# Kernel tuning notes

Hardware: AMD Instinct MI355X
Metric: run time of the kernel (lower is better)

## Reference

```python
import jax, jax.numpy as jnp
import numpy as np

N = 100_000      # nodes
E = 1_600_000    # edges
F_IN = 64        # num_node_features
F = 64           # features_size
OUT = 1          # output_size
V = 2            # variants
A = 6            # activities per variant (second_encoder applied after each)
P = 8192         # (place, src, dst) triples per activity step


def setup_inputs() -> dict:
    key = jax.random.key(0)
    ks = jax.random.split(key, 16)
    s = 1.0 / np.sqrt(F)
    return {
        "x": jax.random.normal(ks[0], (N, F_IN), jnp.float32),
        "edge_index": jax.random.randint(ks[1], (2, E), 0, N, dtype=jnp.int32),
        "places": jax.random.randint(ks[2], (V, A, P), 0, N, dtype=jnp.int32),
        "srcs": jax.random.randint(ks[3], (V, A, P), 0, N, dtype=jnp.int32),
        "dsts": jax.random.randint(ks[4], (V, A, P), 0, N, dtype=jnp.int32),
        "W1": jax.random.normal(ks[5], (F_IN, F), jnp.float32) * s,
        "Wself1": jax.random.normal(ks[6], (F_IN, F), jnp.float32) * s,
        "b1": jnp.zeros((F,), jnp.float32),
        "W2": jax.random.normal(ks[7], (F, F), jnp.float32) * s,
        "Wself2": jax.random.normal(ks[8], (F, F), jnp.float32) * s,
        "b2": jnp.zeros((F,), jnp.float32),
        "Wd1": jax.random.normal(ks[9], (3 * F, F), jnp.float32) * s,
        "bd1": jnp.zeros((F,), jnp.float32),
        "Wd2": jax.random.normal(ks[10], (F, OUT), jnp.float32) * s,
        "bd2": jnp.zeros((OUT,), jnp.float32),
    }


def _gcn(h, edge_src, edge_dst, W, Wself, b):
    # message passing: sum-aggregate neighbor features, then linear + relu
    agg = jax.ops.segment_sum(h[edge_src], edge_dst, num_segments=N)  # [N, F]
    return jax.nn.relu(agg @ W + h @ Wself + b)


def reference(x, edge_index, places, srcs, dsts,
              W1, Wself1, b1, W2, Wself2, b2, Wd1, bd1, Wd2, bd2):
    edge_src, edge_dst = edge_index[0], edge_index[1]

    def decode(feat, p, s, d):
        # gather-concat-MLP-logsigmoid per (place, src, dst) triple
        cat = jnp.concatenate([feat[p], feat[s], feat[d]], axis=-1)  # [P, 3F]
        h = jax.nn.relu(cat @ Wd1 + bd1)
        return jax.nn.log_sigmoid(h @ Wd2 + bd2)                     # [P, OUT]

    feat0 = _gcn(x, edge_src, edge_dst, W1, Wself1, b1)  # first_encoder
    predictions = jnp.zeros((N, OUT), x.dtype)
    for v in range(V):
        feat = feat0  # features reset to post-first-encoder per variant
        pred = jnp.zeros((N, OUT), x.dtype)
        prev_prob = jnp.zeros((OUT,), x.dtype)
        for a in range(A):
            p, s, d = places[v, a], srcs[v, a], dsts[v, a]
            pp = decode(feat, p, s, d)          # [P, OUT]
            pred = pred.at[p].add(pp)           # scatter per place
            prev_prob = prev_prob + pred[p].sum(axis=0)
            pred = pred.at[p].add(prev_prob)    # broadcast to predicted places
            feat = _gcn(feat, edge_src, edge_dst, W2, Wself2, b2)  # second_encoder
        predictions = predictions + pred
    return predictions
```

## Files before the change

kernel.cpp:

```cpp
#include <hip/hip_runtime.h>
#include <hip/hip_bf16.h>

#define F 64
#define VARIANTS 2
#define ACTS 6


__global__ void k_hist(const int* __restrict__ dst, int* __restrict__ deg, int e) {
    int i = blockIdx.x * blockDim.x + threadIdx.x;
    if (i < e) atomicAdd(&deg[dst[i]], 1);
}

__global__ void k_scan1(const int* __restrict__ deg, int* __restrict__ rs,
                        int* __restrict__ bsum, int n) {
    __shared__ int sh[256];
    const int tid = threadIdx.x;
    const int base = blockIdx.x * 1024 + tid * 4;
    int v0 = (base + 0 < n) ? deg[base + 0] : 0;
    int v1 = (base + 1 < n) ? deg[base + 1] : 0;
    int v2 = (base + 2 < n) ? deg[base + 2] : 0;
    int v3 = (base + 3 < n) ? deg[base + 3] : 0;
    const int tsum = v0 + v1 + v2 + v3;
    sh[tid] = tsum;
    __syncthreads();
    for (int off = 1; off < 256; off <<= 1) {
        int t = (tid >= off) ? sh[tid - off] : 0;
        __syncthreads();
        sh[tid] += t;
        __syncthreads();
    }
    int excl = sh[tid] - tsum;
    if (base + 0 < n) rs[base + 0] = excl; excl += v0;
    if (base + 1 < n) rs[base + 1] = excl; excl += v1;
    if (base + 2 < n) rs[base + 2] = excl; excl += v2;
    if (base + 3 < n) rs[base + 3] = excl;
    if (tid == 255) bsum[blockIdx.x] = sh[255];
}

__global__ void k_scan2(int* __restrict__ bsum, int nb) {
    __shared__ int sh[128];
    const int tid = threadIdx.x;
    int v = (tid < nb) ? bsum[tid] : 0;
    sh[tid] = v;
    __syncthreads();
    for (int off = 1; off < 128; off <<= 1) {
        int t = (tid >= off) ? sh[tid - off] : 0;
        __syncthreads();
        sh[tid] += t;
        __syncthreads();
    }
    if (tid < nb) bsum[tid] = sh[tid] - v;
}

__global__ void k_scan3(int* __restrict__ rs, const int* __restrict__ bsum,
                        int* __restrict__ cursor, int n, int total) {
    const int base = blockIdx.x * 1024 + threadIdx.x * 4;
    const int off = bsum[blockIdx.x];
    #pragma unroll
    for (int j = 0; j < 4; ++j) {
        int i = base + j;
        if (i < n) {
            int v = rs[i] + off;
            rs[i] = v;
            cursor[i] = v;
        }
    }
    if (blockIdx.x == 0 && threadIdx.x == 0) rs[n] = total;
}

__global__ void k_fill(const int* __restrict__ src, const int* __restrict__ dst,
                       int* __restrict__ cursor, int* __restrict__ csr, int e0, int e1) {
    int i = e0 + blockIdx.x * blockDim.x + threadIdx.x;
    if (i < e1) {
        int pos = atomicAdd(&cursor[dst[i]], 1);
        csr[pos] = src[i];
    }
}

__global__ __launch_bounds__(256) void k_agg(
    const float* __restrict__ hin, const int* __restrict__ rs,
    const int* __restrict__ csr, float* __restrict__ agg, int n)
{
    const int tid = threadIdx.x;
    const int lane = tid & 63;
    const int nd = blockIdx.x * 4 + (tid >> 6);
    if (nd >= n) return;
    const int beg = rs[nd], end = rs[nd + 1];
    const int sub = lane >> 4;
    const int f4  = lane & 15;
    float ax = 0.f, ay = 0.f, az = 0.f, aw = 0.f;
    for (int cb = beg + sub; cb < end; cb += 4) {
        const int s = csr[cb];
        const float4 v = ((const float4*)(hin + (size_t)s * F))[f4];
        ax += v.x; ay += v.y; az += v.z; aw += v.w;
    }
    #pragma unroll
    for (int o = 16; o <= 32; o <<= 1) {
        ax += __shfl_xor(ax, o);
        ay += __shfl_xor(ay, o);
        az += __shfl_xor(az, o);
        aw += __shfl_xor(aw, o);
    }
    if (sub == 0) {
        float4 r; r.x = ax; r.y = ay; r.z = az; r.w = aw;
        ((float4*)(agg + (size_t)nd * F))[f4] = r;
    }
}

__global__ __launch_bounds__(256) void k_linear(
    const float* __restrict__ agg, const float* __restrict__ hin,
    const float* __restrict__ W, const float* __restrict__ Wself,
    const float* __restrict__ bias, float* __restrict__ out, int n)
{
    const int lane = threadIdx.x & 63;
    const int wv = blockIdx.x * 4 + (threadIdx.x >> 6);
    float wc[64], wsc[64];
    #pragma unroll
    for (int k = 0; k < 64; ++k) {
        wc[k]  = W[k * F + lane];
        wsc[k] = Wself[k * F + lane];
    }
    const float bf = bias[lane];
    const int base = wv * 8;
    #pragma unroll
    for (int t = 0; t < 8; ++t) {
        const int nd = base + t;
        if (nd < n) {
            const float4* __restrict__ ar4 = (const float4*)(agg + (size_t)nd * F);
            const float4* __restrict__ hr4 = (const float4*)(hin + (size_t)nd * F);
            float a = bf;
            #pragma unroll
            for (int q = 0; q < 16; ++q) {
                const float4 v = ar4[q];
                a = fmaf(v.x, wc[q * 4 + 0], a);
                a = fmaf(v.y, wc[q * 4 + 1], a);
                a = fmaf(v.z, wc[q * 4 + 2], a);
                a = fmaf(v.w, wc[q * 4 + 3], a);
            }
            #pragma unroll
            for (int q = 0; q < 16; ++q) {
                const float4 v = hr4[q];
                a = fmaf(v.x, wsc[q * 4 + 0], a);
                a = fmaf(v.y, wsc[q * 4 + 1], a);
                a = fmaf(v.z, wsc[q * 4 + 2], a);
                a = fmaf(v.w, wsc[q * 4 + 3], a);
            }
            out[(size_t)nd * F + lane] = fmaxf(a, 0.f);
        }
    }
}

__global__ __launch_bounds__(256) void k_decode2(
    const float* __restrict__ feat,
    const int* __restrict__ places, const int* __restrict__ srcs, const int* __restrict__ dsts,
    int a, const float* __restrict__ Wd1, const float* __restrict__ bd1,
    const float* __restrict__ Wd2, const float* __restrict__ bd2,
    float* __restrict__ pp_all, int nT, int bpv)
{
    const int v   = blockIdx.x / bpv;
    const int blk = blockIdx.x % bpv;
    const size_t ofs = ((size_t)v * ACTS + a) * nT;
    const int* __restrict__ pi = places + ofs;
    const int* __restrict__ si = srcs   + ofs;
    const int* __restrict__ di = dsts   + ofs;
    float* __restrict__ ppv = pp_all + ofs;

    const int lane = threadIdx.x & 63;
    const int wv = blk * 4 + (threadIdx.x >> 6);
    const int base = wv * 8;
    if (base >= nT) return;
    float acc[8];
    const float b0 = bd1[lane];
    #pragma unroll
    for (int t = 0; t < 8; ++t) acc[t] = b0;

    #pragma unroll
    for (int g = 0; g < 3; ++g) {
        const int* __restrict__ idx = (g == 0) ? pi : (g == 1) ? si : di;
        const float* __restrict__ Wg = Wd1 + (size_t)g * 64 * F;
        float wc[64];
        #pragma unroll
        for (int k = 0; k < 64; ++k) wc[k] = Wg[k * F + lane];
        #pragma unroll
        for (int t = 0; t < 8; ++t) {
            const int tri = base + t;
            if (tri < nT) {
                const int nd = idx[tri];
                const float4* __restrict__ row4 = (const float4*)(feat + (size_t)nd * F);
                float a2 = acc[t];
                #pragma unroll
                for (int q = 0; q < 16; ++q) {
                    const float4 vv = row4[q];
                    a2 = fmaf(vv.x, wc[q * 4 + 0], a2);
                    a2 = fmaf(vv.y, wc[q * 4 + 1], a2);
                    a2 = fmaf(vv.z, wc[q * 4 + 2], a2);
                    a2 = fmaf(vv.w, wc[q * 4 + 3], a2);
                }
                acc[t] = a2;
            }
        }
    }
    const float w2 = Wd2[lane];
    const float b2v = bd2[0];
    #pragma unroll
    for (int t = 0; t < 8; ++t) {
        const int tri = base + t;
        if (tri < nT) {
            float h = fmaxf(acc[t], 0.f);
            float vv = h * w2;
            #pragma unroll
            for (int o = 32; o; o >>= 1) vv += __shfl_xor(vv, o);
            if (lane == 0) {
                float z = vv + b2v;
                ppv[tri] = fminf(z, 0.f) - log1pf(expf(-fabsf(z)));
            }
        }
    }
}

__global__ __launch_bounds__(1024) void k_scatter_all(
    const float* __restrict__ pp_all, const int* __restrict__ places,
    float* __restrict__ pred01, int nP, int strideN)
{
    const int v = blockIdx.x;
    float* __restrict__ pred = pred01 + (size_t)v * strideN;
    __shared__ float wsum[16];
    __shared__ float s_tot;
    __shared__ float s_prev;
    const int tid = threadIdx.x;
    if (tid == 0) s_prev = 0.f;
    __syncthreads();

    for (int a = 0; a < ACTS; ++a) {
        const size_t ofs = ((size_t)v * ACTS + a) * nP;
        const int* __restrict__ p = places + ofs;
        const float* __restrict__ ppv = pp_all + ofs;
        for (int i = tid; i < nP; i += 1024) atomicAdd(&pred[p[i]], ppv[i]);
        __threadfence();
        __syncthreads();
        float s = 0.f;
        for (int i = tid; i < nP; i += 1024)
            s += __hip_atomic_load(&pred[p[i]], __ATOMIC_RELAXED, __HIP_MEMORY_SCOPE_AGENT);
        #pragma unroll
        for (int o = 32; o; o >>= 1) s += __shfl_down(s, o);
        if ((tid & 63) == 0) wsum[tid >> 6] = s;
        __syncthreads();
        if (tid == 0) {
            float tot = 0.f;
            #pragma unroll
            for (int w = 0; w < 16; ++w) tot += wsum[w];
            tot += s_prev;
            s_prev = tot;
            s_tot = tot;
        }
        __syncthreads();
        const float tot = s_tot;
        __threadfence();
        for (int i = tid; i < nP; i += 1024) atomicAdd(&pred[p[i]], tot);
        __threadfence();
        __syncthreads();
    }
}

__global__ void k_sum2(const float* __restrict__ pred01, float* __restrict__ out,
                       int n, int strideN) {
    int i = blockIdx.x * blockDim.x + threadIdx.x;
    if (i < n) out[i] = pred01[i] + pred01[(size_t)strideN + i];
}


extern "C" void kernel_launch(void* const* d_in, const int* in_sizes, int n_in,
                              void* d_out, int out_size, void* d_ws, size_t ws_size,
                              hipStream_t stream) {
    const float* x      = (const float*)d_in[0];
    const int*   eidx   = (const int*)d_in[1];
    const int*   places = (const int*)d_in[2];
    const int*   srcs   = (const int*)d_in[3];
    const int*   dsts   = (const int*)d_in[4];
    const float* W1     = (const float*)d_in[5];
    const float* Wself1 = (const float*)d_in[6];
    const float* b1     = (const float*)d_in[7];
    const float* W2     = (const float*)d_in[8];
    const float* Wself2 = (const float*)d_in[9];
    const float* b2     = (const float*)d_in[10];
    const float* Wd1    = (const float*)d_in[11];
    const float* bd1    = (const float*)d_in[12];
    const float* Wd2    = (const float*)d_in[13];
    const float* bd2    = (const float*)d_in[14];
    float* out          = (float*)d_out;

    const int N = in_sizes[0] / F;
    const int E = in_sizes[1] / 2;
    const int P = in_sizes[2] / (VARIANTS * ACTS);

    const int* edge_src = eidx;
    const int* edge_dst = eidx + E;

    size_t off = 0;
    auto carve = [&](size_t bytes) -> void* {
        void* ptr = (char*)d_ws + off;
        off += (bytes + 255) & ~(size_t)255;
        return ptr;
    };
    int*   deg    = (int*)carve((size_t)N * 4);
    float* pred01 = (float*)carve((size_t)VARIANTS * N * 4);
    const size_t zbytes = off;
    int*   rs     = (int*)carve((size_t)(N + 1) * 4);
    int*   cursor = (int*)carve((size_t)N * 4);
    int*   csr    = (int*)carve((size_t)E * 4);
    int*   bsum   = (int*)carve(128 * 4);
    float* feat0  = (float*)carve((size_t)N * F * 4);
    float* featB  = (float*)carve((size_t)N * F * 4);
    float* featC  = (float*)carve((size_t)N * F * 4);
    float* agg    = (float*)carve((size_t)N * F * 4);
    float* pp_all = (float*)carve((size_t)VARIANTS * ACTS * P * 4);
    (void)ws_size;

    const int nbScan   = (N + 1023) / 1024;
    const int Ehalf    = E / 2;
    const int blkEh    = (Ehalf + 255) / 256;
    const int blkE2    = (E - Ehalf + 255) / 256;
    const int blkAgg   = (N + 3) / 4;
    const int blkLin   = (N + 31) / 32;
    const int bpv      = (P + 31) / 32;
    const int blkAdd   = (N + 255) / 256;

    (void)hipMemsetAsync(d_ws, 0, zbytes, stream);

    k_hist <<<(E + 255) / 256, 256, 0, stream>>>(edge_dst, deg, E);
    k_scan1<<<nbScan, 256, 0, stream>>>(deg, rs, bsum, N);
    k_scan2<<<1, 128, 0, stream>>>(bsum, nbScan);
    k_scan3<<<nbScan, 256, 0, stream>>>(rs, bsum, cursor, N, E);
    k_fill <<<blkEh, 256, 0, stream>>>(edge_src, edge_dst, cursor, csr, 0, Ehalf);
    k_fill <<<blkE2, 256, 0, stream>>>(edge_src, edge_dst, cursor, csr, Ehalf, E);

    k_agg   <<<blkAgg, 256, 0, stream>>>(x, rs, csr, agg, N);
    k_linear<<<blkLin, 256, 0, stream>>>(agg, x, W1, Wself1, b1, feat0, N);

    const float* cur = feat0;
    for (int a = 0; a < ACTS; ++a) {
        k_decode2<<<2 * bpv, 256, 0, stream>>>(cur, places, srcs, dsts, a,
                                               Wd1, bd1, Wd2, bd2, pp_all, P, bpv);
        if (a < ACTS - 1) {
            float* nxt = (cur == featB) ? featC : featB;
            k_agg   <<<blkAgg, 256, 0, stream>>>(cur, rs, csr, agg, N);
            k_linear<<<blkLin, 256, 0, stream>>>(agg, cur, W2, Wself2, b2, nxt, N);
            cur = nxt;
        }
    }
    k_scatter_all<<<VARIANTS, 1024, 0, stream>>>(pp_all, places, pred01, P, N);
    k_sum2<<<blkAdd, 256, 0, stream>>>(pred01, out, N, N);
}
```

Baseline: 1.852 ms.

## Replace sequential per-variant scatter with parallel linear-algebraic decomposition

The serial two-block scatter kernel, which runs six dependent activity steps per variant, is replaced by a decomposition into per-(variant,activity) scatter sums S and place counts c. Small 6x6 interaction matrices are computed in parallel, a tiny kernel resolves the prev_prob recurrence, and a final pass combines everything into the output. This removes the long serial latency of a 1024-thread single-block loop. In exchange it adds about 24 N-sized buffers to zero and read, and the float summation order changes. Feature buffers are also reduced from three to two by reusing feat0.

```diff
diff --git a/kernel.cpp b/kernel.cpp
--- a/kernel.cpp
+++ b/kernel.cpp
@@ -4,6 +4,7 @@
 #define F 64
 #define VARIANTS 2
 #define ACTS 6
+#define NVA (VARIANTS * ACTS)
 
 
 __global__ void k_hist(const int* __restrict__ dst, int* __restrict__ deg, int e) {
@@ -218,54 +219,79 @@
     }
 }
 
-__global__ __launch_bounds__(1024) void k_scatter_all(
-    const float* __restrict__ pp_all, const int* __restrict__ places,
-    float* __restrict__ pred01, int nP, int strideN)
+
+__global__ void k_sc_scatter(const float* __restrict__ pp_all, const int* __restrict__ places,
+                             float* __restrict__ S, float* __restrict__ c, int nP, int n) {
+    int gid = blockIdx.x * blockDim.x + threadIdx.x;
+    if (gid < NVA * nP) {
+        int va = gid / nP;
+        int p = places[gid];
+        atomicAdd(&S[(size_t)va * n + p], pp_all[gid]);
+        atomicAdd(&c[(size_t)va * n + p], 1.0f);
+    }
+}
+
+__global__ __launch_bounds__(256) void k_sc_mats(
+    const float* __restrict__ S, const float* __restrict__ c,
+    const int* __restrict__ places,
+    float* __restrict__ matsA, float* __restrict__ matsC, int nP, int n)
 {
-    const int v = blockIdx.x;
-    float* __restrict__ pred = pred01 + (size_t)v * strideN;
-    __shared__ float wsum[16];
-    __shared__ float s_tot;
-    __shared__ float s_prev;
-    const int tid = threadIdx.x;
-    if (tid == 0) s_prev = 0.f;
+    const int bx = blockIdx.x;
+    const int v = bx / 36;
+    const int a = (bx / 6) % 6;
+    const int b = bx % 6;
+    if (b > a) return;
+    const int* __restrict__ p = places + (size_t)(v * ACTS + a) * nP;
+    const float* __restrict__ Sb = S + (size_t)(v * ACTS + b) * n;
+    const float* __restrict__ cb = c + (size_t)(v * ACTS + b) * n;
+    float sS = 0.f, sC = 0.f;
+    for (int i = threadIdx.x; i < nP; i += 256) {
+        const int idx = p[i];
+        sS += Sb[idx];
+        sC += cb[idx];
+    }
+    __shared__ float shS[4], shC[4];
+    #pragma unroll
+    for (int o = 32; o; o >>= 1) { sS += __shfl_down(sS, o); sC += __shfl_down(sC, o); }
+    const int lane = threadIdx.x & 63, w = threadIdx.x >> 6;
+    if (lane == 0) { shS[w] = sS; shC[w] = sC; }
     __syncthreads();
-
+    if (threadIdx.x == 0) {
+        matsA[bx] = shS[0] + shS[1] + shS[2] + shS[3];
+        matsC[bx] = shC[0] + shC[1] + shC[2] + shC[3];
+    }
+}
+
+__global__ void k_sc_prev(const float* __restrict__ matsA, const float* __restrict__ matsC,
+                          float* __restrict__ prevs) {
+    const int v = threadIdx.x;
+    if (v >= VARIANTS) return;
+    float pl[ACTS];
+    float prev = 0.f;
+    #pragma unroll
     for (int a = 0; a < ACTS; ++a) {
-        const size_t ofs = ((size_t)v * ACTS + a) * nP;
-        const int* __restrict__ p = places + ofs;
-        const float* __restrict__ ppv = pp_all + ofs;
-        for (int i = tid; i < nP; i += 1024) atomicAdd(&pred[p[i]], ppv[i]);
-        __threadfence();
-        __syncthreads();
         float s = 0.f;
-        for (int i = tid; i < nP; i += 1024)
-            s += __hip_atomic_load(&pred[p[i]], __ATOMIC_RELAXED, __HIP_MEMORY_SCOPE_AGENT);
         #pragma unroll
-        for (int o = 32; o; o >>= 1) s += __shfl_down(s, o);
-        if ((tid & 63) == 0) wsum[tid >> 6] = s;
-        __syncthreads();
-        if (tid == 0) {
-            float tot = 0.f;
-            #pragma unroll
-            for (int w = 0; w < 16; ++w) tot += wsum[w];
-            tot += s_prev;
-            s_prev = tot;
-            s_tot = tot;
-        }
-        __syncthreads();
-        const float tot = s_tot;
-        __threadfence();
-        for (int i = tid; i < nP; i += 1024) atomicAdd(&pred[p[i]], tot);
-        __threadfence();
-        __syncthreads();
-    }
-}
-
-__global__ void k_sum2(const float* __restrict__ pred01, float* __restrict__ out,
-                       int n, int strideN) {
+        for (int b = 0; b < ACTS; ++b) {
+            if (b <= a) s += matsA[v * 36 + a * 6 + b];
+            if (b < a)  s += matsC[v * 36 + a * 6 + b] * pl[b];
+        }
+        prev += s;
+        pl[a] = prev;
+        prevs[v * ACTS + a] = prev;
+    }
+}
+
+__global__ void k_out(const float* __restrict__ S, const float* __restrict__ c,
+                      const float* __restrict__ prevs, float* __restrict__ out, int n) {
     int i = blockIdx.x * blockDim.x + threadIdx.x;
-    if (i < n) out[i] = pred01[i] + pred01[(size_t)strideN + i];
+    if (i < n) {
+        float acc = 0.f;
+        #pragma unroll
+        for (int va = 0; va < NVA; ++va)
+            acc += S[(size_t)va * n + i] + c[(size_t)va * n + i] * prevs[va];
+        out[i] = acc;
+    }
 }
 
 
@@ -291,7 +317,7 @@
 
     const int N = in_sizes[0] / F;
     const int E = in_sizes[1] / 2;
-    const int P = in_sizes[2] / (VARIANTS * ACTS);
+    const int P = in_sizes[2] / NVA;
 
     const int* edge_src = eidx;
     const int* edge_dst = eidx + E;
@@ -303,7 +329,8 @@
         return ptr;
     };
     int*   deg    = (int*)carve((size_t)N * 4);
-    float* pred01 = (float*)carve((size_t)VARIANTS * N * 4);
+    float* S      = (float*)carve((size_t)NVA * N * 4);
+    float* c      = (float*)carve((size_t)NVA * N * 4);
     const size_t zbytes = off;
     int*   rs     = (int*)carve((size_t)(N + 1) * 4);
     int*   cursor = (int*)carve((size_t)N * 4);
@@ -311,9 +338,11 @@
     int*   bsum   = (int*)carve(128 * 4);
     float* feat0  = (float*)carve((size_t)N * F * 4);
     float* featB  = (float*)carve((size_t)N * F * 4);
-    float* featC  = (float*)carve((size_t)N * F * 4);
     float* agg    = (float*)carve((size_t)N * F * 4);
-    float* pp_all = (float*)carve((size_t)VARIANTS * ACTS * P * 4);
+    float* pp_all = (float*)carve((size_t)NVA * P * 4);
+    float* matsA  = (float*)carve(72 * 4);
+    float* matsC  = (float*)carve(72 * 4);
+    float* prevs  = (float*)carve(NVA * 4);
     (void)ws_size;
 
     const int nbScan   = (N + 1023) / 1024;
@@ -323,7 +352,7 @@
     const int blkAgg   = (N + 3) / 4;
     const int blkLin   = (N + 31) / 32;
     const int bpv      = (P + 31) / 32;
-    const int blkAdd   = (N + 255) / 256;
+    const int blkN     = (N + 255) / 256;
 
     (void)hipMemsetAsync(d_ws, 0, zbytes, stream);
 
@@ -342,12 +371,15 @@
         k_decode2<<<2 * bpv, 256, 0, stream>>>(cur, places, srcs, dsts, a,
                                                Wd1, bd1, Wd2, bd2, pp_all, P, bpv);
         if (a < ACTS - 1) {
-            float* nxt = (cur == featB) ? featC : featB;
+            float* nxt = (cur == feat0) ? featB : feat0;
             k_agg   <<<blkAgg, 256, 0, stream>>>(cur, rs, csr, agg, N);
             k_linear<<<blkLin, 256, 0, stream>>>(agg, cur, W2, Wself2, b2, nxt, N);
             cur = nxt;
         }
     }
-    k_scatter_all<<<VARIANTS, 1024, 0, stream>>>(pp_all, places, pred01, P, N);
-    k_sum2<<<blkAdd, 256, 0, stream>>>(pred01, out, N, N);
-}
+
+    k_sc_scatter<<<(NVA * P + 255) / 256, 256, 0, stream>>>(pp_all, places, S, c, P, N);
+    k_sc_mats   <<<VARIANTS * 36, 256, 0, stream>>>(S, c, places, matsA, matsC, P, N);
+    k_sc_prev   <<<1, 64, 0, stream>>>(matsA, matsC, prevs);
+    k_out       <<<blkN, 256, 0, stream>>>(S, c, prevs, out, N);
+}
```

Result: faster. 1.597 ms (-13.8%).
